# Optimization experiments

Measured on AMD Instinct MI355X. Metric: run time of the kernel, lower is better.

Reference implementation:

```python
import jax, jax.numpy as jnp
import numpy as np

N, L, E, H = 8, 1024, 512, 4


def setup_inputs() -> dict:
    key = jax.random.key(0)
    ks = jax.random.split(key, 10)
    s = 1.0 / np.sqrt(E)
    return {
        "modalA": jax.random.normal(ks[0], (N, L, E), dtype=jnp.float32),
        "modalB": jax.random.normal(ks[1], (N, L, E), dtype=jnp.float32),
        "WqA": jax.random.normal(ks[2], (E, E), dtype=jnp.float32) * s,
        "bqA": jax.random.normal(ks[3], (E,), dtype=jnp.float32) * s,
        "WkA": jax.random.normal(ks[4], (E, E), dtype=jnp.float32) * s,
        "bkA": jax.random.normal(ks[5], (E,), dtype=jnp.float32) * s,
        "WqB": jax.random.normal(ks[6], (E, E), dtype=jnp.float32) * s,
        "bqB": jax.random.normal(ks[7], (E,), dtype=jnp.float32) * s,
        "WkB": jax.random.normal(ks[8], (E, E), dtype=jnp.float32) * s,
        "bkB": jax.random.normal(ks[9], (E,), dtype=jnp.float32) * s,
    }


def reference(modalA, modalB, WqA, bqA, WkA, bkA, WqB, bqB, WkB, bkB):
    # torch Linear: y = x @ W.T + b
    qA = modalA @ WqA.T + bqA  # [N, L, E]
    kA = modalA @ WkA.T + bkA
    qB = modalB @ WqB.T + bqB
    kB = modalB @ WkB.T + bkB

    # mean over heads of per-head dot products == full-dim dot / num_heads
    # (algebraically identical to einsum('nqhd,nkhd->nhqk').mean(1))
    inv_scale = 1.0 / (H * np.sqrt(E).astype(np.float32))

    def attn(q, k):
        scores = jnp.einsum('nqd,nkd->nqk', q, k) * inv_scale  # [N, L, L]
        return jax.nn.softmax(scores, axis=-1)

    weighted_A = attn(qA, kA)
    weighted_B = attn(qB, kB)
    weighted_AB = attn(qA, kB)
    weighted_BA = attn(qB, kA)

    cat_lower = jnp.concatenate([weighted_A, weighted_AB], axis=-1)  # [N, L, 2L]
    cat_upper = jnp.concatenate([weighted_B, weighted_BA], axis=-1)  # [N, L, 2L]
    cat = jnp.concatenate([cat_lower, cat_upper], axis=1)            # [N, 2L, 2L]
    return jnp.mean(cat, axis=0)                                     # [2L, 2L]
```

## Files before the change

### kernel.cpp

```cpp
#include <hip/hip_runtime.h>
#include <hip/hip_bf16.h>

typedef __bf16 bf16;
typedef bf16 bf16x8 __attribute__((ext_vector_type(8)));
typedef bf16 bf16x4v __attribute__((ext_vector_type(4)));
typedef _Float16 f16;
typedef f16 f16x4 __attribute__((ext_vector_type(4)));
typedef float f32x4 __attribute__((ext_vector_type(4)));

constexpr int LL = 1024;
constexpr int EE = 512;
constexpr int NBATCH = 8;

__device__ __forceinline__ f32x4 mfma16(bf16x8 a, bf16x8 b, f32x4 c) {
    return __builtin_amdgcn_mfma_f32_16x16x32_bf16(a, b, c, 0, 0, 0);
}

#define GLOAD_LDS16(g, l)                                                     \
    __builtin_amdgcn_global_load_lds(                                         \
        (const __attribute__((address_space(1))) void*)(g),                   \
        (__attribute__((address_space(3))) void*)(l), 16, 0, 0)

struct CvtParams {
    const float* src[6];
    bf16* dst[6];
    int n4[6];
};

__global__ __launch_bounds__(256) void cvt_kernel(CvtParams p) {
    const int y = blockIdx.y;
    const float* __restrict__ src = p.src[y];
    bf16* __restrict__ dst = p.dst[y];
    const int n4 = p.n4[y];
    for (int i = blockIdx.x * 256 + threadIdx.x; i < n4; i += gridDim.x * 256) {
        float4 v = *(const float4*)(src + (size_t)i * 4);
        bf16x4v o;
        o[0] = (bf16)v.x; o[1] = (bf16)v.y; o[2] = (bf16)v.z; o[3] = (bf16)v.w;
        *(bf16x4v*)(dst + (size_t)i * 4) = o;
    }
}


struct ProjParams {
    const bf16* x[4];
    const bf16* w[4];
    const float* b[4];
};

__global__ __launch_bounds__(256) void proj_kernel(ProjParams p, bf16* __restrict__ outbase) {
    const int z = blockIdx.z;
    const bf16* __restrict__ X = p.x[z];
    const bf16* __restrict__ W = p.w[z];
    const float* __restrict__ Bv = p.b[z];
    bf16* __restrict__ O = outbase + (size_t)z * (NBATCH * LL) * EE;

    __shared__ union {
        struct { alignas(16) bf16 A[128][32]; alignas(16) bf16 B[128][32]; } st;
        alignas(16) bf16 ep[64][136];
    } sm;

    const int t = threadIdx.x;
    const int lane = t & 63, wid = t >> 6;
    const int wm = wid & 1, wn = wid >> 1;
    const int lr = lane & 15, kg = lane >> 4;
    const int bx = blockIdx.x, by = blockIdx.y;

    f32x4 acc[4][4] = {};

    const int srow = t >> 2;
    const int cgl = t & 3;
    const int gcg = (cgl ^ ((srow >> 1) & 3)) * 8;
    const int scg = (kg ^ ((lr >> 1) & 3)) * 8;

    for (int k0 = 0; k0 < EE; k0 += 32) {
#pragma unroll
        for (int i = 0; i < 2; ++i) {
            const int r = srow + 64 * i;
            GLOAD_LDS16(X + (size_t)(by * 128 + r) * EE + k0 + gcg, &sm.st.A[r][cgl * 8]);
            GLOAD_LDS16(W + (size_t)(bx * 128 + r) * EE + k0 + gcg, &sm.st.B[r][cgl * 8]);
        }
        __builtin_amdgcn_s_waitcnt(0);
        __syncthreads();
        bf16x8 af[4], bfr[4];
#pragma unroll
        for (int im = 0; im < 4; ++im)
            af[im] = *(const bf16x8*)&sm.st.A[wm * 64 + im * 16 + lr][scg];
#pragma unroll
        for (int in = 0; in < 4; ++in)
            bfr[in] = *(const bf16x8*)&sm.st.B[wn * 64 + in * 16 + lr][scg];
#pragma unroll
        for (int im = 0; im < 4; ++im)
#pragma unroll
            for (int in = 0; in < 4; ++in)
                acc[im][in] = mfma16(af[im], bfr[in], acc[im][in]);
        __syncthreads();
    }

#pragma unroll
    for (int pph = 0; pph < 2; ++pph) {
        if (wm == pph) {
#pragma unroll
            for (int im = 0; im < 4; ++im) {
                const int row = im * 16 + kg * 4;
#pragma unroll
                for (int in = 0; in < 4; ++in) {
                    const int col = wn * 64 + in * 16 + lr;
                    const float bias = Bv[bx * 128 + col];
#pragma unroll
                    for (int r = 0; r < 4; ++r)
                        sm.ep[row + r][col] = (bf16)(acc[im][in][r] + bias);
                }
            }
        }
        __syncthreads();
#pragma unroll
        for (int i = 0; i < 4; ++i) {
            const int c = i * 256 + t;
            const int row = c >> 4, colg = (c & 15) * 8;
            *(uint4*)(O + (size_t)(by * 128 + pph * 64 + row) * EE + bx * 128 + colg) =
                *(const uint4*)&sm.ep[row][colg];
        }
        __syncthreads();
    }
}

struct ScoresParams {
    const bf16* q[4];
    const bf16* k[4];
    f16* s[4];
};

__global__ __launch_bounds__(256) void scores_kernel(ScoresParams p) {
    const int f = blockIdx.x + (blockIdx.y << 3) + (blockIdx.z << 6);
    const int xcd = f & 7;
    const int j = f >> 3;
    const int z = (xcd << 2) + (j >> 6);
    const int map = z >> 3, n = z & 7;
    const int tile = j & 63;
    const int bx = tile & 7, by = tile >> 3;

    const bf16* __restrict__ Qb = p.q[map] + (size_t)n * LL * EE;
    const bf16* __restrict__ Kb = p.k[map] + (size_t)n * LL * EE;
    f16* __restrict__ Sb = p.s[map] + (size_t)n * LL * LL;

    __shared__ union {
        struct { alignas(16) bf16 A[128][32]; alignas(16) bf16 B[128][32]; } st;
        alignas(16) f16 ep[64][136];
    } sm;

    const int t = threadIdx.x;
    const int lane = t & 63, wid = t >> 6;
    const int wm = wid & 1, wn = wid >> 1;
    const int lr = lane & 15, kg = lane >> 4;

    f32x4 acc[4][4] = {};

    const int srow = t >> 2;
    const int cgl = t & 3;
    const int gcg = (cgl ^ ((srow >> 1) & 3)) * 8;
    const int scg = (kg ^ ((lr >> 1) & 3)) * 8;

    for (int k0 = 0; k0 < EE; k0 += 32) {
#pragma unroll
        for (int i = 0; i < 2; ++i) {
            const int r = srow + 64 * i;
            GLOAD_LDS16(Qb + (size_t)(by * 128 + r) * EE + k0 + gcg, &sm.st.A[r][cgl * 8]);
            GLOAD_LDS16(Kb + (size_t)(bx * 128 + r) * EE + k0 + gcg, &sm.st.B[r][cgl * 8]);
        }
        __builtin_amdgcn_s_waitcnt(0);
        __syncthreads();
        bf16x8 af[4], bfr[4];
#pragma unroll
        for (int im = 0; im < 4; ++im)
            af[im] = *(const bf16x8*)&sm.st.A[wm * 64 + im * 16 + lr][scg];
#pragma unroll
        for (int in = 0; in < 4; ++in)
            bfr[in] = *(const bf16x8*)&sm.st.B[wn * 64 + in * 16 + lr][scg];
#pragma unroll
        for (int im = 0; im < 4; ++im)
#pragma unroll
            for (int in = 0; in < 4; ++in)
                acc[im][in] = mfma16(af[im], bfr[in], acc[im][in]);
        __syncthreads();
    }

    const float inv_scale = 0.011048543456039806f;
#pragma unroll
    for (int pph = 0; pph < 2; ++pph) {
        if (wm == pph) {
#pragma unroll
            for (int im = 0; im < 4; ++im) {
                const int row = im * 16 + kg * 4;
#pragma unroll
                for (int in = 0; in < 4; ++in) {
                    const int col = wn * 64 + in * 16 + lr;
#pragma unroll
                    for (int r = 0; r < 4; ++r)
                        sm.ep[row + r][col] = (f16)(acc[im][in][r] * inv_scale);
                }
            }
        }
        __syncthreads();
#pragma unroll
        for (int i = 0; i < 4; ++i) {
            const int c = i * 256 + t;
            const int row = c >> 4, colg = (c & 15) * 8;
            *(uint4*)(Sb + (size_t)(by * 128 + pph * 64 + row) * LL + bx * 128 + colg) =
                *(const uint4*)&sm.ep[row][colg];
        }
        __syncthreads();
    }
}

struct SmParams {
    const f16* s[4];
};

__global__ __launch_bounds__(256) void softmax_mean_kernel(SmParams p, float* __restrict__ out) {
    const int q = blockIdx.x;
    const int map = blockIdx.y;
    const f16* __restrict__ S = p.s[map];
    const int t = threadIdx.x;
    const int lane = t & 63, wid = t >> 6;
    __shared__ float red[NBATCH][4];

    f16x4 v[NBATCH];
#pragma unroll
    for (int n = 0; n < NBATCH; ++n)
        v[n] = *(const f16x4*)(S + ((size_t)n * LL + q) * LL + t * 4);

    float e[NBATCH][4];
#pragma unroll
    for (int n = 0; n < NBATCH; ++n) {
        float s = 0.f;
#pragma unroll
        for (int j = 0; j < 4; ++j) {
            e[n][j] = __expf((float)v[n][j]);
            s += e[n][j];
        }
#pragma unroll
        for (int off = 32; off; off >>= 1) s += __shfl_xor(s, off);
        if (lane == 0) red[n][wid] = s;
    }
    __syncthreads();

    float acc[4] = {};
#pragma unroll
    for (int n = 0; n < NBATCH; ++n) {
        const float inv = 1.0f / (red[n][0] + red[n][1] + red[n][2] + red[n][3]);
#pragma unroll
        for (int j = 0; j < 4; ++j) acc[j] += e[n][j] * inv;
    }

    const int orow = (map >= 2 ? LL : 0) + q;
    const int ocol = (map & 1 ? LL : 0) + t * 4;
    float4 o = make_float4(acc[0] * 0.125f, acc[1] * 0.125f, acc[2] * 0.125f, acc[3] * 0.125f);
    *(float4*)(out + (size_t)orow * (2 * LL) + ocol) = o;
}

extern "C" void kernel_launch(void* const* d_in, const int* in_sizes, int n_in,
                              void* d_out, int out_size, void* d_ws, size_t ws_size,
                              hipStream_t stream) {
    const float* modalA = (const float*)d_in[0];
    const float* modalB = (const float*)d_in[1];
    const float* WqA = (const float*)d_in[2];
    const float* bqA = (const float*)d_in[3];
    const float* WkA = (const float*)d_in[4];
    const float* bkA = (const float*)d_in[5];
    const float* WqB = (const float*)d_in[6];
    const float* bqB = (const float*)d_in[7];
    const float* WkB = (const float*)d_in[8];
    const float* bkB = (const float*)d_in[9];
    float* out = (float*)d_out;

    const size_t projN = (size_t)(NBATCH * LL) * EE;
    const size_t mapN = (size_t)NBATCH * LL * LL;
    char* base = (char*)d_ws;
    bf16* qk = (bf16*)base;
    char* region2 = base + 4 * projN * sizeof(bf16);
    bf16* XA = (bf16*)region2;
    bf16* XB = XA + projN;
    bf16* W4 = XB + projN;
    f16* S = (f16*)region2;

    CvtParams cp;
    cp.src[0] = modalA; cp.dst[0] = XA; cp.n4[0] = (int)(projN / 4);
    cp.src[1] = modalB; cp.dst[1] = XB; cp.n4[1] = (int)(projN / 4);
    const float* wsrc[4] = {WqA, WkA, WqB, WkB};
    for (int i = 0; i < 4; ++i) {
        cp.src[2 + i] = wsrc[i];
        cp.dst[2 + i] = W4 + (size_t)i * EE * EE;
        cp.n4[2 + i] = EE * EE / 4;
    }
    cvt_kernel<<<dim3(512, 6), 256, 0, stream>>>(cp);

    ProjParams pp;
    pp.x[0] = XA; pp.x[1] = XA; pp.x[2] = XB; pp.x[3] = XB;
    for (int i = 0; i < 4; ++i) pp.w[i] = W4 + (size_t)i * EE * EE;
    pp.b[0] = bqA; pp.b[1] = bkA; pp.b[2] = bqB; pp.b[3] = bkB;
    proj_kernel<<<dim3(4, 64, 4), 256, 0, stream>>>(pp, qk);

    const bf16* qA = qk + 0 * projN;
    const bf16* kA = qk + 1 * projN;
    const bf16* qB = qk + 2 * projN;
    const bf16* kB = qk + 3 * projN;

    ScoresParams sp;
    sp.q[0] = qA; sp.q[1] = qA; sp.q[2] = qB; sp.q[3] = qB;
    sp.k[0] = kA; sp.k[1] = kB; sp.k[2] = kB; sp.k[3] = kA;
    for (int m = 0; m < 4; ++m) sp.s[m] = S + (size_t)m * mapN;
    scores_kernel<<<dim3(8, 8, 32), 256, 0, stream>>>(sp);

    SmParams smp;
    for (int m = 0; m < 4; ++m) smp.s[m] = S + (size_t)m * mapN;
    softmax_mean_kernel<<<dim3(1024, 4), 256, 0, stream>>>(smp, out);
}
```

Measured before the change: 194.9 us.

## Double-buffer LDS tiles in projection and scores GEMM kernels

Both the projection and the scores GEMM kernels now keep two LDS stages for the A and B tiles. The global-to-LDS load for the next k-slice is issued before the MFMA work on the current slice, and there is one barrier per iteration instead of two. The aim is to hide global load latency behind matrix compute. The cost is double the staging LDS, which may lower occupancy, and the loop is now fully unrolled.

```diff
diff --git a/kernel.cpp b/kernel.cpp
--- a/kernel.cpp
+++ b/kernel.cpp
@@ -55,7 +55,7 @@
     bf16* __restrict__ O = outbase + (size_t)z * (NBATCH * LL) * EE;
 
     __shared__ union {
-        struct { alignas(16) bf16 A[128][32]; alignas(16) bf16 B[128][32]; } st;
+        struct { alignas(16) bf16 A[2][128][32]; alignas(16) bf16 B[2][128][32]; } st;
         alignas(16) bf16 ep[64][136];
     } sm;
 
@@ -72,29 +72,41 @@
     const int gcg = (cgl ^ ((srow >> 1) & 3)) * 8;
     const int scg = (kg ^ ((lr >> 1) & 3)) * 8;
 
-    for (int k0 = 0; k0 < EE; k0 += 32) {
+    const bf16* Xrow0 = X + (size_t)(by * 128 + srow) * EE + gcg;
+    const bf16* Wrow0 = W + (size_t)(bx * 128 + srow) * EE + gcg;
+
+    auto stage = [&](int k, int b) {
+        const int k0 = k * 32;
 #pragma unroll
         for (int i = 0; i < 2; ++i) {
-            const int r = srow + 64 * i;
-            GLOAD_LDS16(X + (size_t)(by * 128 + r) * EE + k0 + gcg, &sm.st.A[r][cgl * 8]);
-            GLOAD_LDS16(W + (size_t)(bx * 128 + r) * EE + k0 + gcg, &sm.st.B[r][cgl * 8]);
-        }
-        __builtin_amdgcn_s_waitcnt(0);
-        __syncthreads();
+            GLOAD_LDS16(Xrow0 + (size_t)(64 * i) * EE + k0, &sm.st.A[b][srow + 64 * i][cgl * 8]);
+            GLOAD_LDS16(Wrow0 + (size_t)(64 * i) * EE + k0, &sm.st.B[b][srow + 64 * i][cgl * 8]);
+        }
+    };
+    auto compute = [&](int b) {
         bf16x8 af[4], bfr[4];
 #pragma unroll
         for (int im = 0; im < 4; ++im)
-            af[im] = *(const bf16x8*)&sm.st.A[wm * 64 + im * 16 + lr][scg];
+            af[im] = *(const bf16x8*)&sm.st.A[b][wm * 64 + im * 16 + lr][scg];
 #pragma unroll
         for (int in = 0; in < 4; ++in)
-            bfr[in] = *(const bf16x8*)&sm.st.B[wn * 64 + in * 16 + lr][scg];
+            bfr[in] = *(const bf16x8*)&sm.st.B[b][wn * 64 + in * 16 + lr][scg];
 #pragma unroll
         for (int im = 0; im < 4; ++im)
 #pragma unroll
             for (int in = 0; in < 4; ++in)
                 acc[im][in] = mfma16(af[im], bfr[in], acc[im][in]);
-        __syncthreads();
-    }
+    };
+
+    stage(0, 0);
+#pragma unroll
+    for (int k = 0; k < 16; ++k) {
+        __builtin_amdgcn_s_waitcnt(0);
+        __syncthreads();
+        if (k < 15) stage(k + 1, (k + 1) & 1);
+        compute(k & 1);
+    }
+    __syncthreads();
 
 #pragma unroll
     for (int pph = 0; pph < 2; ++pph) {
@@ -144,7 +156,7 @@
     f16* __restrict__ Sb = p.s[map] + (size_t)n * LL * LL;
 
     __shared__ union {
-        struct { alignas(16) bf16 A[128][32]; alignas(16) bf16 B[128][32]; } st;
+        struct { alignas(16) bf16 A[2][128][32]; alignas(16) bf16 B[2][128][32]; } st;
         alignas(16) f16 ep[64][136];
     } sm;
 
@@ -160,29 +172,41 @@
     const int gcg = (cgl ^ ((srow >> 1) & 3)) * 8;
     const int scg = (kg ^ ((lr >> 1) & 3)) * 8;
 
-    for (int k0 = 0; k0 < EE; k0 += 32) {
+    const bf16* Qrow0 = Qb + (size_t)(by * 128 + srow) * EE + gcg;
+    const bf16* Krow0 = Kb + (size_t)(bx * 128 + srow) * EE + gcg;
+
+    auto stage = [&](int k, int b) {
+        const int k0 = k * 32;
 #pragma unroll
         for (int i = 0; i < 2; ++i) {
-            const int r = srow + 64 * i;
-            GLOAD_LDS16(Qb + (size_t)(by * 128 + r) * EE + k0 + gcg, &sm.st.A[r][cgl * 8]);
-            GLOAD_LDS16(Kb + (size_t)(bx * 128 + r) * EE + k0 + gcg, &sm.st.B[r][cgl * 8]);
-        }
-        __builtin_amdgcn_s_waitcnt(0);
-        __syncthreads();
+            GLOAD_LDS16(Qrow0 + (size_t)(64 * i) * EE + k0, &sm.st.A[b][srow + 64 * i][cgl * 8]);
+            GLOAD_LDS16(Krow0 + (size_t)(64 * i) * EE + k0, &sm.st.B[b][srow + 64 * i][cgl * 8]);
+        }
+    };
+    auto compute = [&](int b) {
         bf16x8 af[4], bfr[4];
 #pragma unroll
         for (int im = 0; im < 4; ++im)
-            af[im] = *(const bf16x8*)&sm.st.A[wm * 64 + im * 16 + lr][scg];
+            af[im] = *(const bf16x8*)&sm.st.A[b][wm * 64 + im * 16 + lr][scg];
 #pragma unroll
         for (int in = 0; in < 4; ++in)
-            bfr[in] = *(const bf16x8*)&sm.st.B[wn * 64 + in * 16 + lr][scg];
+            bfr[in] = *(const bf16x8*)&sm.st.B[b][wn * 64 + in * 16 + lr][scg];
 #pragma unroll
         for (int im = 0; im < 4; ++im)
 #pragma unroll
             for (int in = 0; in < 4; ++in)
                 acc[im][in] = mfma16(af[im], bfr[in], acc[im][in]);
-        __syncthreads();
-    }
+    };
+
+    stage(0, 0);
+#pragma unroll
+    for (int k = 0; k < 16; ++k) {
+        __builtin_amdgcn_s_waitcnt(0);
+        __syncthreads();
+        if (k < 15) stage(k + 1, (k + 1) & 1);
+        compute(k & 1);
+    }
+    __syncthreads();
 
     const float inv_scale = 0.011048543456039806f;
 #pragma unroll
```

New measurement: 189.1 us. -3.0%, faster.
